# Kernel optimization log

Hardware: AMD Instinct MI355X
Metric: run time of the kernel (lower is better)

## Reference

```python
import jax, jax.numpy as jnp
import numpy as np
import math

B, S, E, H, F, V, L = 2, 2048, 1024, 16, 4096, 32000, 2
D = E // H
START = 1
EPS = 1e-6


def setup_inputs() -> dict:
    key = jax.random.key(0)
    ks = jax.random.split(key, 16)
    k_emb = 1.0 / math.sqrt(V)
    std = 0.02
    inp = {
        "tokens": jax.random.randint(ks[0], (B, S), 0, V),
        "word_embed": jax.random.normal(ks[1], (V, E), jnp.float32) * k_emb,
        "pos_embed": jax.random.normal(ks[2], (S, E), jnp.float32) * k_emb,
        "unembed_b": jnp.zeros((V,), jnp.float32),
        "kqv_w": jax.random.normal(ks[3], (L, 3 * E, E), jnp.float32) * std,
        "wo_w": jax.random.normal(ks[4], (L, E, E), jnp.float32) * std,
        "up_w": jax.random.normal(ks[5], (L, F, E), jnp.float32) * std,
        "up_b": jnp.zeros((L, F), jnp.float32),
        "down_w": jax.random.normal(ks[6], (L, E, F), jnp.float32) * std,
        "down_b": jnp.zeros((L, E), jnp.float32),
        "ln1_s": jnp.ones((L, E), jnp.float32),
        "ln1_b": jnp.zeros((L, E), jnp.float32),
        "ln2_s": jnp.ones((L, E), jnp.float32),
        "ln2_b": jnp.zeros((L, E), jnp.float32),
    }
    return inp


def _layer_norm(x, scale, bias):
    m = jnp.mean(x, axis=-1, keepdims=True)
    v = jnp.var(x, axis=-1, keepdims=True)  # biased, matches torch LayerNorm
    return (x - m) / jnp.sqrt(v + EPS) * scale + bias


def _causal_block_mask(tokens):
    # block-diagonal segments split at START tokens, plus causal triu
    is_start = tokens == START
    seg = jnp.cumsum(is_start, axis=1)  # [B,S]
    block = seg[:, :, None] != seg[:, None, :]  # [B,S,S]
    triu = jnp.triu(jnp.ones((S, S), bool), k=1)
    return triu[None, :, :] | block  # [B,S,S], True = masked


def _resetting_positions(tokens):
    is_start = tokens == START
    is_start = is_start.at[:, 0].set(True)
    pos = jnp.arange(S)
    start_pos = jnp.where(is_start, pos[None, :], 0)
    last_start = jax.lax.cummax(start_pos, axis=1)
    return pos[None, :] - last_start  # [B,S]


def reference(tokens, word_embed, pos_embed, unembed_b, kqv_w, wo_w,
              up_w, up_b, down_w, down_b, ln1_s, ln1_b, ln2_s, ln2_b):
    mask = _causal_block_mask(tokens)[:, None, :, :]  # [B,1,S,S]
    rel_pos = _resetting_positions(tokens)
    x = word_embed[tokens] + pos_embed[rel_pos]  # [B,S,E]
    scale = 1.0 / math.sqrt(D)

    for l in range(L):
        # attention
        qkv = (x @ kqv_w[l].T).reshape(B, S, 3, H, D)
        k, q, v = qkv[:, :, 0], qkv[:, :, 1], qkv[:, :, 2]  # [B,S,H,D]
        attn = jnp.einsum('bqhd,bkhd->bhqk', q, k) * scale
        attn = jnp.where(mask, -jnp.inf, attn)
        attn = jax.nn.softmax(attn, axis=-1)
        out = jnp.einsum('bhqk,bkhd->bqhd', attn, v).reshape(B, S, E)
        out = out @ wo_w[l].T
        x = _layer_norm(out + x, ln1_s[l], ln1_b[l])
        # FFN
        h = jax.nn.relu(x @ up_w[l].T + up_b[l])
        h = h @ down_w[l].T + down_b[l]
        x = _layer_norm(h + x, ln2_s[l], ln2_b[l])

    # weight-tied unembed
    logits = x @ word_embed.T + unembed_b  # [B,S,V]
    return logits
```

## Files before the change

kernel.cpp:

```cpp
#include <hip/hip_runtime.h>
#include <hip/hip_bf16.h>

#define BB 2
#define SS 2048
#define EE 1024
#define HH 16
#define DD 64
#define FF 4096
#define VV 32000
#define LL 2
#define BS (BB*SS)

#define NEG_HUGE (-3.402823466e+38f)

typedef __attribute__((ext_vector_type(4)))  float  f32x4;
typedef __attribute__((ext_vector_type(16))) float  f32x16;
typedef __attribute__((ext_vector_type(8)))  __bf16 bf16x8;
typedef __attribute__((ext_vector_type(4)))  __bf16 bf16x4;

__device__ inline bf16x8 to_bf8(float4 a, float4 b) {
  bf16x8 r;
  r[0] = (__bf16)a.x; r[1] = (__bf16)a.y; r[2] = (__bf16)a.z; r[3] = (__bf16)a.w;
  r[4] = (__bf16)b.x; r[5] = (__bf16)b.y; r[6] = (__bf16)b.z; r[7] = (__bf16)b.w;
  return r;
}

typedef const unsigned int __attribute__((address_space(1)))* gptr_t;
typedef unsigned int __attribute__((address_space(3)))* lptr_t;
__device__ inline void gload16(const void* g, void* l) {
  __builtin_amdgcn_global_load_lds((gptr_t)g, (lptr_t)l, 16, 0, 0);
}

__global__ __launch_bounds__(1024) void lastart_scan(
    const int* __restrict__ tokens, int* __restrict__ ls) {
  __shared__ int buf[SS];
  const int b = blockIdx.x, t = threadIdx.x;
#pragma unroll
  for (int j = 0; j < 2; ++j) {
    int i = t + j * 1024;
    buf[i] = (i > 0 && tokens[b*SS + i] == 1) ? i : 0;
  }
  __syncthreads();
  for (int off = 1; off < SS; off <<= 1) {
    int i0 = t, i1 = t + 1024;
    int v0 = (i0 >= off) ? max(buf[i0], buf[i0 - off]) : buf[i0];
    int v1 = (i1 >= off) ? max(buf[i1], buf[i1 - off]) : buf[i1];
    __syncthreads();
    buf[i0] = v0; buf[i1] = v1;
    __syncthreads();
  }
#pragma unroll
  for (int j = 0; j < 2; ++j) {
    int i = t + j * 1024;
    ls[b*SS + i] = buf[i];
  }
}

__global__ __launch_bounds__(256) void embed_kernel(
    const int* __restrict__ tokens, const int* __restrict__ ls,
    const float* __restrict__ we, const float* __restrict__ pe,
    float* __restrict__ x, __bf16* __restrict__ xb) {
  int row = blockIdx.x;
  int s = row & (SS - 1);
  int tok = tokens[row];
  int rp = s - ls[row];
  const float4* w4 = (const float4*)(we + (size_t)tok * EE);
  const float4* p4 = (const float4*)(pe + (size_t)rp * EE);
  float4 a = w4[threadIdx.x];
  float4 b = p4[threadIdx.x];
  float4 o; o.x = a.x + b.x; o.y = a.y + b.y; o.z = a.z + b.z; o.w = a.w + b.w;
  ((float4*)(x + (size_t)row * EE))[threadIdx.x] = o;
  bf16x4 ob4;
  ob4[0] = (__bf16)o.x; ob4[1] = (__bf16)o.y; ob4[2] = (__bf16)o.z; ob4[3] = (__bf16)o.w;
  *(bf16x4*)(xb + (size_t)row * EE + threadIdx.x * 4) = ob4;
}

__global__ __launch_bounds__(256) void cvt_bf16_kernel(
    const float* __restrict__ src, __bf16* __restrict__ dst, int n) {
  int i = (blockIdx.x * 256 + threadIdx.x) * 8;
  if (i + 8 > n) return;
  float4 a = *(const float4*)(src + i);
  float4 b = *(const float4*)(src + i + 4);
  *(bf16x8*)(dst + i) = to_bf8(a, b);
}

__device__ inline void stage_half8(const __bf16* __restrict__ base,
                                   __bf16* region, int K, int kofs,
                                   int col8, int srow, int sdst) {
#pragma unroll
  for (int p = 0; p < 2; ++p)
    gload16(base + (size_t)(p * 128 + srow) * K + kofs + col8,
            region + p * 4096 + sdst);
}

template<int NMT, bool BIAS, bool RELU, bool OUTBF16>
__global__ __launch_bounds__(512, 2) void gemm_8ph(
    const __bf16* __restrict__ A, const __bf16* __restrict__ W,
    const float* __restrict__ bias, void* __restrict__ Cv,
    int N, int K, int nmg) {
  __shared__ __bf16 lds[8][8192];
  const int t = threadIdx.x, l = t & 63, w = t >> 6;
  const int nwg = gridDim.x, orig = blockIdx.x;
  const int q = nwg >> 3, r = nwg & 7, xcd = orig & 7, pos = orig >> 3;
  const int wgid = (xcd < r ? xcd*(q+1) : r*(q+1) + (xcd-r)*q) + pos;
  const int mgrp = wgid % nmg, n0 = (wgid / nmg) * 256;
  const int wm = w >> 2, wn = w & 3;
  const int fr = l & 15, c8 = l >> 4;
  const int swz = (c8 ^ ((fr >> 1) & 3)) * 8;
  const int roA = (wm*128 + fr) * 32 + swz;
  const int roB = (wn*64  + fr) * 32 + swz;
  const int col8 = ((t & 3) ^ ((t >> 3) & 3)) * 8;
  const int srow = t >> 2;
  const int sdst = (t >> 6) * 512;

  const __bf16* Wb = W + (size_t)n0 * K;
  const int ng = NMT * 16;

  float bv[4];
#pragma unroll
  for (int j = 0; j < 4; ++j) bv[j] = BIAS ? bias[n0 + wn*64 + fr + j*16] : 0.0f;

  f32x4 acc[8][4] = {};

#define ABASE(g2) (A + (size_t)(mgrp*NMT + ((g2) >> 4)) * 256 * K)
#define KOFS(g2)  (((g2) & 15) * 64)

  stage_half8(ABASE(0), &lds[0][0], K, 0,  col8, srow, sdst);
  stage_half8(Wb,       &lds[2][0], K, 0,  col8, srow, sdst);
  stage_half8(ABASE(0), &lds[1][0], K, 32, col8, srow, sdst);
  stage_half8(Wb,       &lds[3][0], K, 32, col8, srow, sdst);
  stage_half8(ABASE(1), &lds[4][0], K, 64, col8, srow, sdst);
  stage_half8(Wb,       &lds[6][0], K, 64, col8, srow, sdst);
  asm volatile("s_waitcnt vmcnt(4)" ::: "memory");
  __builtin_amdgcn_s_barrier();

  for (int g = 0; g < ng; ++g) {
    const int c = g & 1;
    const int rA = c*4, rB = c*4 + 2;
    bf16x8 afr[4], bfr[4];
#pragma unroll
    for (int j = 0; j < 4; ++j) bfr[j] = *(const bf16x8*)&lds[rB][roB + j*512];
#pragma unroll
    for (int i = 0; i < 4; ++i) afr[i] = *(const bf16x8*)&lds[rA][roA + i*512];
    if (g + 1 < ng)
      stage_half8(ABASE(g+1), &lds[(c^1)*4 + 1][0], K, KOFS(g+1) + 32, col8, srow, sdst);
    __builtin_amdgcn_s_barrier();
    __builtin_amdgcn_s_setprio(1);
#pragma unroll
    for (int i = 0; i < 4; ++i)
#pragma unroll
      for (int j = 0; j < 4; ++j)
        acc[i][j] = __builtin_amdgcn_mfma_f32_16x16x32_bf16(afr[i], bfr[j], acc[i][j], 0, 0, 0);
    __builtin_amdgcn_s_setprio(0);
    __builtin_amdgcn_s_barrier();
#pragma unroll
    for (int i = 0; i < 4; ++i) afr[i] = *(const bf16x8*)&lds[rA][roA + (i+4)*512];
    if (g + 1 < ng)
      stage_half8(Wb, &lds[(c^1)*4 + 3][0], K, KOFS(g+1) + 32, col8, srow, sdst);
    __builtin_amdgcn_s_barrier();
    __builtin_amdgcn_s_setprio(1);
#pragma unroll
    for (int i = 0; i < 4; ++i)
#pragma unroll
      for (int j = 0; j < 4; ++j)
        acc[i+4][j] = __builtin_amdgcn_mfma_f32_16x16x32_bf16(afr[i], bfr[j], acc[i+4][j], 0, 0, 0);
    __builtin_amdgcn_s_setprio(0);
    if (g < ng - 1) { asm volatile("s_waitcnt vmcnt(8)" ::: "memory"); }
    else            { asm volatile("s_waitcnt vmcnt(0)" ::: "memory"); }
    __builtin_amdgcn_s_barrier();
#pragma unroll
    for (int j = 0; j < 4; ++j) bfr[j] = *(const bf16x8*)&lds[rB + 1][roB + j*512];
#pragma unroll
    for (int i = 0; i < 4; ++i) afr[i] = *(const bf16x8*)&lds[rA + 1][roA + i*512];
    if (g + 2 < ng)
      stage_half8(ABASE(g+2), &lds[c*4][0], K, KOFS(g+2), col8, srow, sdst);
    __builtin_amdgcn_s_barrier();
    __builtin_amdgcn_s_setprio(1);
#pragma unroll
    for (int i = 0; i < 4; ++i)
#pragma unroll
      for (int j = 0; j < 4; ++j)
        acc[i][j] = __builtin_amdgcn_mfma_f32_16x16x32_bf16(afr[i], bfr[j], acc[i][j], 0, 0, 0);
    __builtin_amdgcn_s_setprio(0);
    __builtin_amdgcn_s_barrier();
#pragma unroll
    for (int i = 0; i < 4; ++i) afr[i] = *(const bf16x8*)&lds[rA + 1][roA + (i+4)*512];
    if (g + 2 < ng)
      stage_half8(Wb, &lds[c*4 + 2][0], K, KOFS(g+2), col8, srow, sdst);
    __builtin_amdgcn_s_barrier();
    __builtin_amdgcn_s_setprio(1);
#pragma unroll
    for (int i = 0; i < 4; ++i)
#pragma unroll
      for (int j = 0; j < 4; ++j)
        acc[i+4][j] = __builtin_amdgcn_mfma_f32_16x16x32_bf16(afr[i], bfr[j], acc[i+4][j], 0, 0, 0);
    __builtin_amdgcn_s_setprio(0);
    if (g < ng - 2)       { asm volatile("s_waitcnt vmcnt(8)" ::: "memory"); }
    else if (g == ng - 2) { asm volatile("s_waitcnt vmcnt(4)" ::: "memory"); }
    __builtin_amdgcn_s_barrier();
    if ((g & 15) == 15) {
      const int orow = (mgrp*NMT + (g >> 4)) * 256 + wm*128 + c8 * 4;
      const int ocol = n0 + wn*64 + fr;
#pragma unroll
      for (int i = 0; i < 8; ++i)
#pragma unroll
        for (int j = 0; j < 4; ++j) {
#pragma unroll
          for (int rr = 0; rr < 4; ++rr) {
            float v = acc[i][j][rr] + bv[j];
            if (RELU) v = fmaxf(v, 0.0f);
            if (OUTBF16)
              ((__bf16*)Cv)[(size_t)(orow + i*16 + rr) * N + ocol + j*16] = (__bf16)v;
            else
              ((float*)Cv)[(size_t)(orow + i*16 + rr) * N + ocol + j*16] = v;
          }
          acc[i][j] = (f32x4){};
        }
    }
  }
#undef ABASE
#undef KOFS
}

template<int T, int BM>
__device__ inline void stage2(const __bf16* __restrict__ Ab,
                              const __bf16* __restrict__ Wb,
                              __bf16* la, __bf16* lb, int K, int k0, int t) {
  const int col8 = (t & 3) ^ ((t >> 3) & 3);
  const int cofs = k0 + col8 * 8;
  const int wbase = (t >> 6) * 512;
#pragma unroll
  for (int p = 0; p < (BM * 32) / (T * 8); ++p) {
    const int row = p * (T >> 2) + (t >> 2);
    gload16(Ab + (size_t)row * K + cofs, la + p * T * 8 + wbase);
    gload16(Wb + (size_t)row * K + cofs, lb + p * T * 8 + wbase);
  }
}

template<int RW, int WM, int WN, bool BIAS, bool RELU, bool OUTBF16>
__global__ __launch_bounds__(WM*WN*64, 2) void gemm_deep(
    const __bf16* __restrict__ A, const __bf16* __restrict__ W,
    const float* __restrict__ bias, void* __restrict__ Cv,
    int N, int K, int nbx) {
  constexpr int T  = WM * WN * 64;
  constexpr int BM = WM * RW * 16;
  __shared__ __bf16 lds[4][2][BM * 32];
  const int t = threadIdx.x, l = t & 63, w = t >> 6;
  const int nwg = gridDim.x, orig = blockIdx.x;
  const int q = nwg >> 3, r = nwg & 7, xcd = orig & 7, pos = orig >> 3;
  const int wgid = (xcd < r ? xcd*(q+1) : r*(q+1) + (xcd-r)*q) + pos;
  const int m0 = (wgid % nbx) * BM, n0 = (wgid / nbx) * BM;
  const int wm = w / WN, wn = w % WN;
  const int fr = l & 15, c8 = l >> 4;
  const int slot = (c8 ^ ((fr >> 1) & 3)) * 8;

  const __bf16* Abase = A + (size_t)m0 * K;
  const __bf16* Wbase = W + (size_t)n0 * K;

  f32x4 acc[RW][4] = {};

  const int nk = K >> 5;
  stage2<T,BM>(Abase, Wbase, &lds[0][0][0], &lds[0][1][0], K, 0,  t);
  stage2<T,BM>(Abase, Wbase, &lds[1][0][0], &lds[1][1][0], K, 32, t);
  stage2<T,BM>(Abase, Wbase, &lds[2][0][0], &lds[2][1][0], K, 64, t);

  for (int kt = 0; kt < nk; ++kt) {
    const int cur = kt & 3;
    if (kt + 3 < nk) {
      const int nb = (kt + 3) & 3;
      stage2<T,BM>(Abase, Wbase, &lds[nb][0][0], &lds[nb][1][0], K, (kt+3)*32, t);
      asm volatile("s_waitcnt vmcnt(8)" ::: "memory");
    } else if (kt + 2 < nk) {
      asm volatile("s_waitcnt vmcnt(8)" ::: "memory");
    } else if (kt + 1 < nk) {
      asm volatile("s_waitcnt vmcnt(4)" ::: "memory");
    } else {
      asm volatile("s_waitcnt vmcnt(0)" ::: "memory");
    }
    __builtin_amdgcn_s_barrier();
    __builtin_amdgcn_sched_barrier(0);
    const __bf16* La = &lds[cur][0][0];
    const __bf16* Lb = &lds[cur][1][0];
    bf16x8 bfr[4];
#pragma unroll
    for (int j = 0; j < 4; ++j)
      bfr[j] = *(const bf16x8*)&Lb[(wn*64 + j*16 + fr) * 32 + slot];
    __builtin_amdgcn_s_setprio(1);
#pragma unroll
    for (int i = 0; i < RW; ++i) {
      bf16x8 af = *(const bf16x8*)&La[(wm*(RW*16) + i*16 + fr) * 32 + slot];
#pragma unroll
      for (int j = 0; j < 4; ++j)
        acc[i][j] = __builtin_amdgcn_mfma_f32_16x16x32_bf16(af, bfr[j], acc[i][j], 0, 0, 0);
    }
    __builtin_amdgcn_s_setprio(0);
    __builtin_amdgcn_sched_barrier(0);
    __builtin_amdgcn_s_barrier();
    __builtin_amdgcn_sched_barrier(0);
  }

  const int orow = m0 + wm*(RW*16) + c8 * 4;
  const int ocol = n0 + wn*64 + fr;
#pragma unroll
  for (int i = 0; i < RW; ++i)
#pragma unroll
    for (int j = 0; j < 4; ++j) {
      const int col = ocol + j * 16;
      const float bv = BIAS ? bias[col] : 0.0f;
#pragma unroll
      for (int rr = 0; rr < 4; ++rr) {
        float v = acc[i][j][rr] + bv;
        if (RELU) v = fmaxf(v, 0.0f);
        if (OUTBF16)
          ((__bf16*)Cv)[(size_t)(orow + i*16 + rr) * N + col] = (__bf16)v;
        else
          ((float*)Cv)[(size_t)(orow + i*16 + rr) * N + col] = v;
      }
    }
}

template<bool WBF16, bool BIAS, bool RELU, bool OUTBF16>
__global__ __launch_bounds__(256) void gemm_fast(
    const __bf16* __restrict__ A, const void* __restrict__ Wv,
    const float* __restrict__ bias, void* __restrict__ Cv, int N, int K) {
  __shared__ __bf16 As[128][32];
  __shared__ __bf16 Bs[128][32];
  const int t = threadIdx.x;
  const int m0 = blockIdx.x * 128, n0 = blockIdx.y * 128;
  const int l = t & 63, w = t >> 6;
  const int wm = (w >> 1) * 64, wn = (w & 1) * 64;
  const int fr = l & 15, fk = (l >> 4) * 8;
  const int crow = l >> 2, ccol = (l & 3) * 8;
  const int wrow = t >> 1, wcol = (t & 1) * 16;

  const __bf16* Wb = (const __bf16*)Wv;
  const float*  Wf = (const float*)Wv;

  f32x4 acc[4][4] = {};

  for (int k0 = 0; k0 < K; k0 += 32) {
    float4 wf0, wf1, wf2, wf3;
    if (!WBF16) {
      const float* wp = Wf + (size_t)(n0 + wrow) * K + k0 + wcol;
      wf0 = *(const float4*)(wp);
      wf1 = *(const float4*)(wp + 4);
      wf2 = *(const float4*)(wp + 8);
      wf3 = *(const float4*)(wp + 12);
    }
    __syncthreads();
#pragma unroll
    for (int i = 0; i < 2; ++i) {
      const int c = 2 * w + i;
      gload16(A + (size_t)(m0 + c*16 + crow) * K + k0 + ccol, (__bf16*)As + c*512);
      if (WBF16)
        gload16(Wb + (size_t)(n0 + c*16 + crow) * K + k0 + ccol, (__bf16*)Bs + c*512);
    }
    if (!WBF16) {
      *(bf16x8*)&Bs[wrow][wcol]     = to_bf8(wf0, wf1);
      *(bf16x8*)&Bs[wrow][wcol + 8] = to_bf8(wf2, wf3);
    }
    __syncthreads();
    bf16x8 af[4], bf[4];
#pragma unroll
    for (int i = 0; i < 4; ++i) af[i] = *(const bf16x8*)&As[wm + i*16 + fr][fk];
#pragma unroll
    for (int j = 0; j < 4; ++j) bf[j] = *(const bf16x8*)&Bs[wn + j*16 + fr][fk];
#pragma unroll
    for (int i = 0; i < 4; ++i)
#pragma unroll
      for (int j = 0; j < 4; ++j)
        acc[i][j] = __builtin_amdgcn_mfma_f32_16x16x32_bf16(af[i], bf[j], acc[i][j], 0, 0, 0);
  }

  const int orow = m0 + wm + (l >> 4) * 4;
  const int ocol = n0 + wn + fr;
#pragma unroll
  for (int i = 0; i < 4; ++i)
#pragma unroll
    for (int j = 0; j < 4; ++j) {
      const int col = ocol + j * 16;
      const float bv = BIAS ? bias[col] : 0.0f;
#pragma unroll
      for (int r = 0; r < 4; ++r) {
        float v = acc[i][j][r] + bv;
        if (RELU) v = fmaxf(v, 0.0f);
        if (OUTBF16)
          ((__bf16*)Cv)[(size_t)(orow + i*16 + r) * N + col] = (__bf16)v;
        else
          ((float*)Cv)[(size_t)(orow + i*16 + r) * N + col] = v;
      }
    }
}

__global__ __launch_bounds__(256) void ln_res_kernel(
    const float* __restrict__ y, float* __restrict__ x, __bf16* __restrict__ xb,
    const float* __restrict__ sc, const float* __restrict__ bs) {
  __shared__ float red[8];
  int row = blockIdx.x, t = threadIdx.x;
  const float4* y4 = (const float4*)(y + (size_t)row * EE);
  float4* x4 = (float4*)(x + (size_t)row * EE);
  float4 a = y4[t], c = x4[t];
  float v0 = a.x + c.x, v1 = a.y + c.y, v2 = a.z + c.z, v3 = a.w + c.w;
  float s = v0 + v1 + v2 + v3;
  float q = v0*v0 + v1*v1 + v2*v2 + v3*v3;
#pragma unroll
  for (int off = 32; off; off >>= 1) {
    s += __shfl_xor(s, off);
    q += __shfl_xor(q, off);
  }
  int w = t >> 6;
  if ((t & 63) == 0) { red[w] = s; red[4 + w] = q; }
  __syncthreads();
  s = red[0] + red[1] + red[2] + red[3];
  q = red[4] + red[5] + red[6] + red[7];
  float mean = s * (1.0f / EE);
  float var  = q * (1.0f / EE) - mean * mean;
  float r = 1.0f / sqrtf(var + 1e-6f);
  float4 ss = ((const float4*)sc)[t];
  float4 bb = ((const float4*)bs)[t];
  float4 o;
  o.x = (v0 - mean) * r * ss.x + bb.x;
  o.y = (v1 - mean) * r * ss.y + bb.y;
  o.z = (v2 - mean) * r * ss.z + bb.z;
  o.w = (v3 - mean) * r * ss.w + bb.w;
  x4[t] = o;
  bf16x4 ob4;
  ob4[0] = (__bf16)o.x; ob4[1] = (__bf16)o.y; ob4[2] = (__bf16)o.z; ob4[3] = (__bf16)o.w;
  *(bf16x4*)(xb + (size_t)row * EE + t * 4) = ob4;
}

__global__ __launch_bounds__(256) void attn_mfma(
    const __bf16* __restrict__ qkv, const int* __restrict__ ls,
    __bf16* __restrict__ out) {
  const int id = blockIdx.x;
  const int z = id >> 8, rem = id & 255;
  const int qt0 = rem & 15, h = rem >> 4, b = z;
  const int qt = z ? (15 - qt0) : qt0;
  __shared__ f32x4 lds4[2304];
  char* lds = (char*)lds4;
  __bf16* Ks = (__bf16*)lds;
  __bf16* Vs = (__bf16*)(lds + 9216);
  __shared__ int redmin[4];
  const int t = threadIdx.x, w = t >> 6, l = t & 63;
  __bf16* Pq = (__bf16*)(lds + 18432 + w * 4608);
  const int r = l & 31, hi = l >> 5;
  const int qb = qt * 128, qw = qb + w * 32, qg = qw + r;
  const int Lq = ls[b*SS + qg];

  {
    int mn = Lq;
#pragma unroll
    for (int off = 1; off < 64; off <<= 1) mn = min(mn, __shfl_xor(mn, off));
    if (l == 0) redmin[w] = mn;
  }

  bf16x8 qf[4];
  {
    const __bf16* qrow = qkv + (size_t)(b*SS + qg) * 3*EE + EE + h*DD + 8*hi;
#pragma unroll
    for (int ds = 0; ds < 4; ++ds) qf[ds] = *(const bf16x8*)(qrow + 16*ds);
  }
  __syncthreads();
  const int ktmin = min(min(redmin[0], redmin[1]), min(redmin[2], redmin[3])) >> 6;
  const int ktmax = 2*qt + 1;

  f32x16 oacc[2] = {};
  float m_r = NEG_HUGE, lsum = 0.0f;

  for (int kt = ktmin; kt <= ktmax; ++kt) {
    __syncthreads();
    {
      const int kr = t >> 2, c0 = (t & 3) * 16;
      const __bf16* kg = qkv + (size_t)(b*SS + kt*64 + kr) * 3*EE + h*DD + c0;
      const __bf16* vg = kg + 2*EE;
      bf16x8 k0 = *(const bf16x8*)kg;
      bf16x8 k1 = *(const bf16x8*)(kg + 8);
      bf16x8 v0 = *(const bf16x8*)vg;
      bf16x8 v1 = *(const bf16x8*)(vg + 8);
      *(bf16x8*)&Ks[kr*72 + c0]     = k0;
      *(bf16x8*)&Ks[kr*72 + c0 + 8] = k1;
      const int vc = (kr + 8*(t & 3)) & 63;
#pragma unroll
      for (int j = 0; j < 8; ++j) {
        Vs[(c0 + j)*72 + vc]     = v0[j];
        Vs[(c0 + 8 + j)*72 + vc] = v1[j];
      }
    }
    __syncthreads();

    bool act0 = (kt*64)      <= (qw + 31);
    bool act1 = (kt*64 + 32) <= (qw + 31);
    if (!act0) continue;

    f32x16 st[2];
    st[0] = (f32x16){};
    st[1] = (f32x16){};
#pragma unroll
    for (int ds = 0; ds < 4; ++ds) {
      bf16x8 kf = *(const bf16x8*)&Ks[(r)*72 + 16*ds + 8*hi];
      st[0] = __builtin_amdgcn_mfma_f32_32x32x16_bf16(kf, qf[ds], st[0], 0, 0, 0);
    }
    if (act1) {
#pragma unroll
      for (int ds = 0; ds < 4; ++ds) {
        bf16x8 kf = *(const bf16x8*)&Ks[(32 + r)*72 + 16*ds + 8*hi];
        st[1] = __builtin_amdgcn_mfma_f32_32x32x16_bf16(kf, qf[ds], st[1], 0, 0, 0);
      }
    }

    float tmax = NEG_HUGE;
#pragma unroll
    for (int kt2 = 0; kt2 < 2; ++kt2) {
#pragma unroll
      for (int reg = 0; reg < 16; ++reg) {
        const int key = kt*64 + 32*kt2 + (reg & 3) + 8*(reg >> 2) + 4*hi;
        float s = (kt2 == 0 || act1) ? st[kt2][reg] * 0.125f : NEG_HUGE;
        const bool valid = (key >= Lq) && (key <= qg);
        s = valid ? s : NEG_HUGE;
        st[kt2][reg] = s;
        tmax = fmaxf(tmax, s);
      }
    }
    tmax = fmaxf(tmax, __shfl_xor(tmax, 32));
    const float m_new = fmaxf(m_r, tmax);
    const float alpha = __expf(m_r - m_new);
    m_r = m_new;

    float psum = 0.0f;
#pragma unroll
    for (int kt2 = 0; kt2 < 2; ++kt2) {
#pragma unroll
      for (int g2 = 0; g2 < 4; ++g2) {
        bf16x4 pk;
#pragma unroll
        for (int j = 0; j < 4; ++j) {
          float p = __expf(st[kt2][g2*4 + j] - m_new);
          psum += p;
          pk[j] = (__bf16)p;
        }
        *(bf16x4*)&Pq[r*72 + 32*kt2 + 8*g2 + 4*hi] = pk;
      }
    }
    psum += __shfl_xor(psum, 32);
    lsum = lsum * alpha + psum;
    oacc[0] *= alpha;
    oacc[1] *= alpha;

#pragma unroll
    for (int ks = 0; ks < 4; ++ks) {
      if (kt*64 + 16*ks > qw + 31) continue;
      bf16x8 pf = *(const bf16x8*)&Pq[r*72 + 16*ks + 8*hi];
#pragma unroll
      for (int mt = 0; mt < 2; ++mt) {
        const int d = 32*mt + r;
        const int vcol = (16*ks + 8*hi + 8*((d >> 4) & 3)) & 63;
        bf16x8 vf = *(const bf16x8*)&Vs[d*72 + vcol];
        oacc[mt] = __builtin_amdgcn_mfma_f32_32x32x16_bf16(vf, pf, oacc[mt], 0, 0, 0);
      }
    }
  }

  __syncthreads();
  float* Ot = (float*)(lds + w * 8448);
  const float rinv = 1.0f / lsum;
#pragma unroll
  for (int mt = 0; mt < 2; ++mt)
#pragma unroll
    for (int reg = 0; reg < 16; ++reg) {
      const int d = 32*mt + (reg & 3) + 8*(reg >> 2) + 4*hi;
      Ot[d*33 + r] = oacc[mt][reg] * rinv;
    }
  __syncthreads();
  const int qr0 = l >> 4, dc = (l & 15) * 4;
#pragma unroll
  for (int it = 0; it < 8; ++it) {
    const int qr = qr0 + 4*it;
    bf16x4 ov;
    ov[0] = (__bf16)Ot[(dc+0)*33 + qr];
    ov[1] = (__bf16)Ot[(dc+1)*33 + qr];
    ov[2] = (__bf16)Ot[(dc+2)*33 + qr];
    ov[3] = (__bf16)Ot[(dc+3)*33 + qr];
    *(bf16x4*)(out + (size_t)(b*SS + qw + qr) * EE + h*DD + dc) = ov;
  }
}

extern "C" void kernel_launch(void* const* d_in, const int* in_sizes, int n_in,
                              void* d_out, int out_size, void* d_ws, size_t ws_size,
                              hipStream_t stream) {
  const int*   tokens     = (const int*)  d_in[0];
  const float* word_embed = (const float*)d_in[1];
  const float* pos_embed  = (const float*)d_in[2];
  const float* unembed_b  = (const float*)d_in[3];
  const float* kqv_w      = (const float*)d_in[4];
  const float* wo_w       = (const float*)d_in[5];
  const float* up_w       = (const float*)d_in[6];
  const float* up_b       = (const float*)d_in[7];
  const float* down_w     = (const float*)d_in[8];
  const float* down_b     = (const float*)d_in[9];
  const float* ln1_s      = (const float*)d_in[10];
  const float* ln1_b      = (const float*)d_in[11];
  const float* ln2_s      = (const float*)d_in[12];
  const float* ln2_b      = (const float*)d_in[13];
  float* logits = (float*)d_out;

  char* ob = (char*)d_out;
  __bf16* qkv  = (__bf16*)ob;
  __bf16* t0   = (__bf16*)(ob +  24ull*1024*1024);
  __bf16* hbuf = (__bf16*)(ob +  32ull*1024*1024);
  float*  ybuf = (float*) (ob +  64ull*1024*1024);
  __bf16* wcvt = (__bf16*)(ob +  80ull*1024*1024);
  float*  x    = (float*) (ob + 131ull*1024*1024);
  __bf16* kqvb  = wcvt;
  __bf16* wob   = kqvb + (size_t)LL*3*EE*EE;
  __bf16* upb   = wob  + (size_t)LL*EE*EE;
  __bf16* downb = upb  + (size_t)LL*FF*EE;
  int*    ls   = (int*)d_ws;
  __bf16* xb   = (__bf16*)((char*)d_ws + 65536);
  __bf16* webf = (__bf16*)((char*)d_ws + 65536 + 8ull*1024*1024);
  const bool bigws = ws_size >= (size_t)(65536 + 8ull*1024*1024 + (size_t)VV*EE*2);

  lastart_scan<<<BB, 1024, 0, stream>>>(tokens, ls);
  embed_kernel<<<BS, 256, 0, stream>>>(tokens, ls, word_embed, pos_embed, x, xb);

  cvt_bf16_kernel<<<LL*3*EE*EE/2048, 256, 0, stream>>>(kqv_w,  kqvb,  LL*3*EE*EE);
  cvt_bf16_kernel<<<LL*EE*EE/2048,   256, 0, stream>>>(wo_w,   wob,   LL*EE*EE);
  cvt_bf16_kernel<<<LL*FF*EE/2048,   256, 0, stream>>>(up_w,   upb,   LL*FF*EE);
  cvt_bf16_kernel<<<LL*EE*FF/2048,   256, 0, stream>>>(down_w, downb, LL*EE*FF);
  if (bigws)
    cvt_bf16_kernel<<<VV*EE/2048, 256, 0, stream>>>(word_embed, webf, VV*EE);

  for (int l = 0; l < LL; ++l) {
    gemm_8ph<1,false,false,true><<<(BS/256)*(3*EE/256), 512, 0, stream>>>(
        xb, kqvb + (size_t)l*3*EE*EE, nullptr, qkv, 3*EE, EE, BS/256);
    attn_mfma<<<512, 256, 0, stream>>>(qkv, ls, t0);
    gemm_deep<4,2,2,false,false,false><<<(BS/128)*(EE/128), 256, 0, stream>>>(
        t0, wob + (size_t)l*EE*EE, nullptr, ybuf, EE, EE, BS/128);
    ln_res_kernel<<<BS, 256, 0, stream>>>(ybuf, x, xb, ln1_s + l*EE, ln1_b + l*EE);
    gemm_8ph<1,true,true,true><<<(BS/256)*(FF/256), 512, 0, stream>>>(
        xb, upb + (size_t)l*FF*EE, up_b + (size_t)l*FF, hbuf, FF, EE, BS/256);
    gemm_deep<4,2,2,true,false,false><<<(BS/128)*(EE/128), 256, 0, stream>>>(
        hbuf, downb + (size_t)l*EE*FF, down_b + (size_t)l*EE, ybuf, EE, FF, BS/128);
    ln_res_kernel<<<BS, 256, 0, stream>>>(ybuf, x, xb, ln2_s + l*EE, ln2_b + l*EE);
  }

  if (bigws) {
    gemm_8ph<8,true,false,false><<<(VV/256)*2, 512, 0, stream>>>(
        xb, webf, unembed_b, logits, VV, EE, 2);
  } else {
    gemm_fast<false,true,false,false><<<dim3(BS/128, VV/128), 256, 0, stream>>>(
        xb, word_embed, unembed_b, logits, VV, EE);
  }
}
```

Baseline: 897.1 us.

## Preload A fragments, emit bf16 GEMM outputs, and shrink attention blocks

Three unrelated changes. The 8-phase GEMM now loads both halves of the A fragments from LDS up front instead of reloading between MFMA phases. The Wo and down-projection GEMMs write bf16 instead of fp32 and the layernorm reads bf16, which halves that intermediate traffic at the cost of rounding the residual input. Attention now runs 1024 blocks of 128 threads over 64-row query tiles with a smaller LDS footprint and wider per-thread K/V staging, to improve occupancy and load balance.

```diff
diff --git a/kernel.cpp b/kernel.cpp
--- a/kernel.cpp
+++ b/kernel.cpp
@@ -137,11 +137,13 @@
   for (int g = 0; g < ng; ++g) {
     const int c = g & 1;
     const int rA = c*4, rB = c*4 + 2;
-    bf16x8 afr[4], bfr[4];
-#pragma unroll
-    for (int j = 0; j < 4; ++j) bfr[j] = *(const bf16x8*)&lds[rB][roB + j*512];
-#pragma unroll
-    for (int i = 0; i < 4; ++i) afr[i] = *(const bf16x8*)&lds[rA][roA + i*512];
+    bf16x8 afr0[4], afr1[4], bfr[4];
+#pragma unroll
+    for (int j = 0; j < 4; ++j) bfr[j]  = *(const bf16x8*)&lds[rB][roB + j*512];
+#pragma unroll
+    for (int i = 0; i < 4; ++i) afr0[i] = *(const bf16x8*)&lds[rA][roA + i*512];
+#pragma unroll
+    for (int i = 0; i < 4; ++i) afr1[i] = *(const bf16x8*)&lds[rA][roA + (i+4)*512];
     if (g + 1 < ng)
       stage_half8(ABASE(g+1), &lds[(c^1)*4 + 1][0], K, KOFS(g+1) + 32, col8, srow, sdst);
     __builtin_amdgcn_s_barrier();
@@ -150,11 +152,9 @@
     for (int i = 0; i < 4; ++i)
 #pragma unroll
       for (int j = 0; j < 4; ++j)
-        acc[i][j] = __builtin_amdgcn_mfma_f32_16x16x32_bf16(afr[i], bfr[j], acc[i][j], 0, 0, 0);
+        acc[i][j] = __builtin_amdgcn_mfma_f32_16x16x32_bf16(afr0[i], bfr[j], acc[i][j], 0, 0, 0);
     __builtin_amdgcn_s_setprio(0);
     __builtin_amdgcn_s_barrier();
-#pragma unroll
-    for (int i = 0; i < 4; ++i) afr[i] = *(const bf16x8*)&lds[rA][roA + (i+4)*512];
     if (g + 1 < ng)
       stage_half8(Wb, &lds[(c^1)*4 + 3][0], K, KOFS(g+1) + 32, col8, srow, sdst);
     __builtin_amdgcn_s_barrier();
@@ -163,15 +163,17 @@
     for (int i = 0; i < 4; ++i)
 #pragma unroll
       for (int j = 0; j < 4; ++j)
-        acc[i+4][j] = __builtin_amdgcn_mfma_f32_16x16x32_bf16(afr[i], bfr[j], acc[i+4][j], 0, 0, 0);
+        acc[i+4][j] = __builtin_amdgcn_mfma_f32_16x16x32_bf16(afr1[i], bfr[j], acc[i+4][j], 0, 0, 0);
     __builtin_amdgcn_s_setprio(0);
     if (g < ng - 1) { asm volatile("s_waitcnt vmcnt(8)" ::: "memory"); }
     else            { asm volatile("s_waitcnt vmcnt(0)" ::: "memory"); }
     __builtin_amdgcn_s_barrier();
 #pragma unroll
-    for (int j = 0; j < 4; ++j) bfr[j] = *(const bf16x8*)&lds[rB + 1][roB + j*512];
-#pragma unroll
-    for (int i = 0; i < 4; ++i) afr[i] = *(const bf16x8*)&lds[rA + 1][roA + i*512];
+    for (int j = 0; j < 4; ++j) bfr[j]  = *(const bf16x8*)&lds[rB + 1][roB + j*512];
+#pragma unroll
+    for (int i = 0; i < 4; ++i) afr0[i] = *(const bf16x8*)&lds[rA + 1][roA + i*512];
+#pragma unroll
+    for (int i = 0; i < 4; ++i) afr1[i] = *(const bf16x8*)&lds[rA + 1][roA + (i+4)*512];
     if (g + 2 < ng)
       stage_half8(ABASE(g+2), &lds[c*4][0], K, KOFS(g+2), col8, srow, sdst);
     __builtin_amdgcn_s_barrier();
@@ -180,11 +182,9 @@
     for (int i = 0; i < 4; ++i)
 #pragma unroll
       for (int j = 0; j < 4; ++j)
-        acc[i][j] = __builtin_amdgcn_mfma_f32_16x16x32_bf16(afr[i], bfr[j], acc[i][j], 0, 0, 0);
+        acc[i][j] = __builtin_amdgcn_mfma_f32_16x16x32_bf16(afr0[i], bfr[j], acc[i][j], 0, 0, 0);
     __builtin_amdgcn_s_setprio(0);
     __builtin_amdgcn_s_barrier();
-#pragma unroll
-    for (int i = 0; i < 4; ++i) afr[i] = *(const bf16x8*)&lds[rA + 1][roA + (i+4)*512];
     if (g + 2 < ng)
       stage_half8(Wb, &lds[c*4 + 2][0], K, KOFS(g+2), col8, srow, sdst);
     __builtin_amdgcn_s_barrier();
@@ -193,7 +193,7 @@
     for (int i = 0; i < 4; ++i)
 #pragma unroll
       for (int j = 0; j < 4; ++j)
-        acc[i+4][j] = __builtin_amdgcn_mfma_f32_16x16x32_bf16(afr[i], bfr[j], acc[i+4][j], 0, 0, 0);
+        acc[i+4][j] = __builtin_amdgcn_mfma_f32_16x16x32_bf16(afr1[i], bfr[j], acc[i+4][j], 0, 0, 0);
     __builtin_amdgcn_s_setprio(0);
     if (g < ng - 2)       { asm volatile("s_waitcnt vmcnt(8)" ::: "memory"); }
     else if (g == ng - 2) { asm volatile("s_waitcnt vmcnt(4)" ::: "memory"); }
@@ -393,14 +393,15 @@
 }
 
 __global__ __launch_bounds__(256) void ln_res_kernel(
-    const float* __restrict__ y, float* __restrict__ x, __bf16* __restrict__ xb,
+    const __bf16* __restrict__ y, float* __restrict__ x, __bf16* __restrict__ xb,
     const float* __restrict__ sc, const float* __restrict__ bs) {
   __shared__ float red[8];
   int row = blockIdx.x, t = threadIdx.x;
-  const float4* y4 = (const float4*)(y + (size_t)row * EE);
+  bf16x4 a4 = *(const bf16x4*)(y + (size_t)row * EE + t * 4);
   float4* x4 = (float4*)(x + (size_t)row * EE);
-  float4 a = y4[t], c = x4[t];
-  float v0 = a.x + c.x, v1 = a.y + c.y, v2 = a.z + c.z, v3 = a.w + c.w;
+  float4 c = x4[t];
+  float v0 = (float)a4[0] + c.x, v1 = (float)a4[1] + c.y;
+  float v2 = (float)a4[2] + c.z, v3 = (float)a4[3] + c.w;
   float s = v0 + v1 + v2 + v3;
   float q = v0*v0 + v1*v1 + v2*v2 + v3*v3;
 #pragma unroll
@@ -429,22 +430,23 @@
   *(bf16x4*)(xb + (size_t)row * EE + t * 4) = ob4;
 }
 
-__global__ __launch_bounds__(256) void attn_mfma(
+__global__ __launch_bounds__(128) void attn_mfma(
     const __bf16* __restrict__ qkv, const int* __restrict__ ls,
     __bf16* __restrict__ out) {
   const int id = blockIdx.x;
-  const int z = id >> 8, rem = id & 255;
-  const int qt0 = rem & 15, h = rem >> 4, b = z;
-  const int qt = z ? (15 - qt0) : qt0;
-  __shared__ f32x4 lds4[2304];
+  const int b  = id >> 9;
+  const int h  = (id >> 5) & 15;
+  const int q0 = id & 31;
+  const int qt2 = ((id >> 5) & 1) ? 31 - q0 : q0;
+  __shared__ f32x4 lds4[1728];
   char* lds = (char*)lds4;
   __bf16* Ks = (__bf16*)lds;
   __bf16* Vs = (__bf16*)(lds + 9216);
-  __shared__ int redmin[4];
+  __shared__ int redmin[2];
   const int t = threadIdx.x, w = t >> 6, l = t & 63;
   __bf16* Pq = (__bf16*)(lds + 18432 + w * 4608);
   const int r = l & 31, hi = l >> 5;
-  const int qb = qt * 128, qw = qb + w * 32, qg = qw + r;
+  const int qb = qt2 * 64, qw = qb + w * 32, qg = qw + r;
   const int Lq = ls[b*SS + qg];
 
   {
@@ -461,8 +463,8 @@
     for (int ds = 0; ds < 4; ++ds) qf[ds] = *(const bf16x8*)(qrow + 16*ds);
   }
   __syncthreads();
-  const int ktmin = min(min(redmin[0], redmin[1]), min(redmin[2], redmin[3])) >> 6;
-  const int ktmax = 2*qt + 1;
+  const int ktmin = min(redmin[0], redmin[1]) >> 6;
+  const int ktmax = qt2;
 
   f32x16 oacc[2] = {};
   float m_r = NEG_HUGE, lsum = 0.0f;
@@ -470,20 +472,30 @@
   for (int kt = ktmin; kt <= ktmax; ++kt) {
     __syncthreads();
     {
-      const int kr = t >> 2, c0 = (t & 3) * 16;
-      const __bf16* kg = qkv + (size_t)(b*SS + kt*64 + kr) * 3*EE + h*DD + c0;
+      const int kr = t >> 1, ch = (t & 1) * 32;
+      const __bf16* kg = qkv + (size_t)(b*SS + kt*64 + kr) * 3*EE + h*DD + ch;
       const __bf16* vg = kg + 2*EE;
       bf16x8 k0 = *(const bf16x8*)kg;
       bf16x8 k1 = *(const bf16x8*)(kg + 8);
+      bf16x8 k2 = *(const bf16x8*)(kg + 16);
+      bf16x8 k3 = *(const bf16x8*)(kg + 24);
       bf16x8 v0 = *(const bf16x8*)vg;
       bf16x8 v1 = *(const bf16x8*)(vg + 8);
-      *(bf16x8*)&Ks[kr*72 + c0]     = k0;
-      *(bf16x8*)&Ks[kr*72 + c0 + 8] = k1;
-      const int vc = (kr + 8*(t & 3)) & 63;
+      bf16x8 v2 = *(const bf16x8*)(vg + 16);
+      bf16x8 v3 = *(const bf16x8*)(vg + 24);
+      *(bf16x8*)&Ks[kr*72 + ch]      = k0;
+      *(bf16x8*)&Ks[kr*72 + ch + 8]  = k1;
+      *(bf16x8*)&Ks[kr*72 + ch + 16] = k2;
+      *(bf16x8*)&Ks[kr*72 + ch + 24] = k3;
+      const int g0 = ch >> 4;
+      const int vc0 = (kr + 8*(g0 & 3)) & 63;
+      const int vc1 = (kr + 8*((g0 + 1) & 3)) & 63;
 #pragma unroll
       for (int j = 0; j < 8; ++j) {
-        Vs[(c0 + j)*72 + vc]     = v0[j];
-        Vs[(c0 + 8 + j)*72 + vc] = v1[j];
+        Vs[(ch + j)*72      + vc0] = v0[j];
+        Vs[(ch + 8 + j)*72  + vc0] = v1[j];
+        Vs[(ch + 16 + j)*72 + vc1] = v2[j];
+        Vs[(ch + 24 + j)*72 + vc1] = v3[j];
       }
     }
     __syncthreads();
@@ -607,7 +619,7 @@
   __bf16* qkv  = (__bf16*)ob;
   __bf16* t0   = (__bf16*)(ob +  24ull*1024*1024);
   __bf16* hbuf = (__bf16*)(ob +  32ull*1024*1024);
-  float*  ybuf = (float*) (ob +  64ull*1024*1024);
+  __bf16* ybuf = (__bf16*)(ob +  64ull*1024*1024);
   __bf16* wcvt = (__bf16*)(ob +  80ull*1024*1024);
   float*  x    = (float*) (ob + 131ull*1024*1024);
   __bf16* kqvb  = wcvt;
@@ -632,13 +644,13 @@
   for (int l = 0; l < LL; ++l) {
     gemm_8ph<1,false,false,true><<<(BS/256)*(3*EE/256), 512, 0, stream>>>(
         xb, kqvb + (size_t)l*3*EE*EE, nullptr, qkv, 3*EE, EE, BS/256);
-    attn_mfma<<<512, 256, 0, stream>>>(qkv, ls, t0);
-    gemm_deep<4,2,2,false,false,false><<<(BS/128)*(EE/128), 256, 0, stream>>>(
+    attn_mfma<<<1024, 128, 0, stream>>>(qkv, ls, t0);
+    gemm_deep<4,2,2,false,false,true><<<(BS/128)*(EE/128), 256, 0, stream>>>(
         t0, wob + (size_t)l*EE*EE, nullptr, ybuf, EE, EE, BS/128);
     ln_res_kernel<<<BS, 256, 0, stream>>>(ybuf, x, xb, ln1_s + l*EE, ln1_b + l*EE);
     gemm_8ph<1,true,true,true><<<(BS/256)*(FF/256), 512, 0, stream>>>(
         xb, upb + (size_t)l*FF*EE, up_b + (size_t)l*FF, hbuf, FF, EE, BS/256);
-    gemm_deep<4,2,2,true,false,false><<<(BS/128)*(EE/128), 256, 0, stream>>>(
+    gemm_deep<4,2,2,true,false,true><<<(BS/128)*(EE/128), 256, 0, stream>>>(
         hbuf, downb + (size_t)l*EE*FF, down_b + (size_t)l*EE, ybuf, EE, FF, BS/128);
     ln_res_kernel<<<BS, 256, 0, stream>>>(ybuf, x, xb, ln2_s + l*EE, ln2_b + l*EE);
   }
```

New measurement: 927.3 us. +3.4%, slower.
